# Optimization experiments

Measured on AMD Instinct MI355X. Metric: run time of the kernel, lower is better.

Reference implementation:

```python
import jax, jax.numpy as jnp
import numpy as np

N = 8192
N_DIM = 7
N_WIDTH = 64


def setup_inputs() -> dict:
    key = jax.random.key(0)
    ks = jax.random.split(key, 12)
    scale = 0.05
    u = lambda k, shape: scale * (2.0 * jax.random.uniform(k, shape) - 1.0)
    # Linear params stored as (in, out) so forward uses x @ W + b (same math as torch Linear).
    lin = lambda k, fan_in, fan_out: (
        jax.random.uniform(jax.random.fold_in(k, 0), (fan_in, fan_out),
                           minval=-1.0, maxval=1.0) / np.sqrt(fan_in),
        jax.random.uniform(jax.random.fold_in(k, 1), (fan_out,),
                           minval=-1.0, maxval=1.0) / np.sqrt(fan_in),
    )
    W1, b1 = lin(ks[1], N_DIM, N_WIDTH)
    W2, b2 = lin(ks[2], N_WIDTH, N_WIDTH)
    Wl, bl = lin(ks[3], N_WIDTH, 1)
    return {
        "x": jax.random.normal(ks[0], (N, N_DIM), dtype=jnp.float32),
        "alpha": jax.random.uniform(ks[4], (1,)),          # Edges.alpha = 1 * rand(1)
        "W1": W1, "b1": b1, "wt1": u(ks[5], (N_WIDTH, N_WIDTH)), "bs1": u(ks[6], (1,)),
        "W2": W2, "b2": b2, "wt2": u(ks[7], (N_WIDTH, N_WIDTH)), "bs2": u(ks[8], (1,)),
        "Wl": Wl, "bl": bl,
    }


def _edges(x, alpha):
    eta, phi = x[:, 1], x[:, 2]
    deta = eta[:, None] - eta[None, :]                      # (n, n)
    dphi = jnp.abs(phi[:, None] - phi[None, :])
    dphi = jnp.where(dphi > jnp.pi, 2.0 * jnp.pi - dphi, dphi)
    dRdR = deta * deta + dphi * dphi
    A = jnp.exp(-alpha[0] * dRdR)
    return jax.nn.softmax(A, axis=1) + jnp.eye(x.shape[0], dtype=x.dtype)


def _gcn_layer(X, A, W, b, wt, bs):
    X = jax.nn.relu(X @ W + b)                              # embed + relu
    X = (A @ X) @ wt + bs[0]                                # aggregate + mix + scalar bias
    return jax.nn.relu(X)


def reference(x, alpha, W1, b1, wt1, bs1, W2, b2, wt2, bs2, Wl, bl):
    A = _edges(x, alpha)
    V = jax.nn.relu(_gcn_layer(x, A, W1, b1, wt1, bs1))
    V = jax.nn.relu(_gcn_layer(V, A, W2, b2, wt2, bs2))
    s = V.sum(axis=0)                                       # (n_width,)
    return jax.nn.sigmoid(s @ Wl + bl)                      # (1,)
```

## Files before the change

### kernel.cpp

```cpp
#include <hip/hip_runtime.h>
#include <math.h>

#define NN 8192
#define L2E 1.44269504088896340736f
#define TWO_PI 6.28318530717958647693f

typedef _Float16 h8 __attribute__((ext_vector_type(8)));
typedef _Float16 h4 __attribute__((ext_vector_type(4)));
typedef float f32x4 __attribute__((ext_vector_type(4)));
#define MFMA16(A, B, C) __builtin_amdgcn_mfma_f32_16x16x32_f16(A, B, C, 0, 0, 0)

#define GLD_LDS16(gsrc, ldst)                                          \
  __builtin_amdgcn_global_load_lds(                                    \
      (const __attribute__((address_space(1))) unsigned int*)(gsrc),   \
      (__attribute__((address_space(3))) unsigned int*)(ldst), 16, 0, 0)

union V8 { float4 v[2]; float f[8]; };

__global__ __launch_bounds__(256) void prep_kernel(
    const float* __restrict__ x, const float* __restrict__ alpha,
    const float* __restrict__ W1, const float* __restrict__ b1,
    float* __restrict__ eta_s, float* __restrict__ phi_s,
    float* __restrict__ H1, _Float16* __restrict__ HT1,
    float* __restrict__ svec)
{
  __shared__ float sW[448];
  __shared__ float sb[64];
  __shared__ float T[32][65];
  const int t = threadIdx.x;
  if (blockIdx.x == 0 && t < 64) svec[t] = 0.f;
  for (int k = t; k < 448; k += 256) sW[k] = W1[k];
  if (t < 64) sb[t] = b1[t];
  const float s = sqrtf(alpha[0] * L2E);
  const int i0 = blockIdx.x * 32;
  const int r = t >> 3, q = t & 7;
  const int i = i0 + r;
  float xv[7];
#pragma unroll
  for (int k = 0; k < 7; k++) xv[k] = x[i * 7 + k];
  if (q == 0) { eta_s[i] = xv[1] * s; phi_s[i] = xv[2] * s; }
  __syncthreads();
#pragma unroll
  for (int c = 0; c < 8; c++) {
    const int n = q * 8 + c;
    float hv = sb[n];
#pragma unroll
    for (int k = 0; k < 7; k++) hv = fmaf(xv[k], sW[k * 64 + n], hv);
    T[r][n] = fmaxf(hv, 0.f);
  }
  __syncthreads();
  for (int e = t; e < 2048; e += 256) H1[i0 * 64 + e] = T[e >> 6][e & 63];
  const int n = t >> 2, sg = (t & 3) * 8;
  h8 v;
#pragma unroll
  for (int ss = 0; ss < 8; ss++) v[ss] = (_Float16)T[sg + ss][n];
  *(h8*)(HT1 + (size_t)n * NN + i0 + sg) = v;
}

template <bool NEED_L>
__global__ __launch_bounds__(256, 4) void attn_pass(
    const float* __restrict__ eta_s, const float* __restrict__ phi_s,
    const _Float16* __restrict__ HT, const float* __restrict__ alpha,
    float* __restrict__ Ypart, float* __restrict__ lpart)
{
  __shared__ __align__(16) char smem[33792];
  _Float16* stage = (_Float16*)smem;
  const int tid = threadIdx.x;
  const int w = tid >> 6, lane = tid & 63, m = lane & 15, g = lane >> 4;
  const int tile = blockIdx.x >> 2, part = blockIdx.x & 3;
  const int i0 = tile << 5;
  const int jbase = part << 11;
  const float Cs = TWO_PI * sqrtf(alpha[0] * L2E);
  const float et0 = eta_s[i0 + m],      ph0 = phi_s[i0 + m];
  const float et1 = eta_s[i0 + 16 + m], ph1 = phi_s[i0 + 16 + m];

  const int r0 = tid >> 4, gq = tid & 15;
  const _Float16* sbase = HT + (size_t)r0 * NN + ((gq ^ r0) << 3) + jbase;

  f32x4 a00 = {0,0,0,0}, a01 = {0,0,0,0}, a02 = {0,0,0,0}, a03 = {0,0,0,0};
  f32x4 a10 = {0,0,0,0}, a11 = {0,0,0,0}, a12 = {0,0,0,0}, a13 = {0,0,0,0};
  float l0 = 0.f, l1 = 0.f;

  const float* ep = eta_s + jbase + (w << 5) + (g << 3);
  const float* pp = phi_s + jbase + (w << 5) + (g << 3);
  V8 E, P, En, Pn;
  E.v[0] = *(const float4*)ep;  E.v[1] = *(const float4*)(ep + 4);
  P.v[0] = *(const float4*)pp;  P.v[1] = *(const float4*)(pp + 4);
  En = E; Pn = P;

#pragma unroll
  for (int k = 0; k < 4; ++k)
    GLD_LDS16(sbase + (size_t)k * 16 * NN, stage + ((k * 256 + tid) << 3));
  __syncthreads();

  const int fs = ((m << 4) + (((w << 2) | g) ^ m)) << 3;

  union AF { h8 v; decltype(__builtin_amdgcn_cvt_pkrtz(0.f, 0.f)) p[4]; };

  for (int s = 0; s < 16; ++s) {
    _Float16* cur = stage + ((s & 1) << 13);
    if (s < 15) {
      _Float16* nxt = stage + (((s + 1) & 1) << 13);
      const _Float16* srcp = sbase + (s + 1) * 128;
#pragma unroll
      for (int k = 0; k < 4; ++k)
        GLD_LDS16(srcp + (size_t)k * 16 * NN, nxt + ((k * 256 + tid) << 3));
      En.v[0] = *(const float4*)(ep + 128); En.v[1] = *(const float4*)(ep + 132);
      Pn.v[0] = *(const float4*)(pp + 128); Pn.v[1] = *(const float4*)(pp + 132);
      ep += 128; pp += 128;
    }
    const h8 b0 = *(const h8*)(cur + fs);
    const h8 b1 = *(const h8*)(cur + 2048 + fs);
    const h8 b2 = *(const h8*)(cur + 4096 + fs);
    const h8 b3 = *(const h8*)(cur + 6144 + fs);

    AF af0, af1;
#pragma unroll
    for (int tt = 0; tt < 8; tt += 2) {
      float Pv[4];
#pragma unroll
      for (int u = 0; u < 2; ++u) {
        {
          const float dp = ph0 - P.f[tt + u];
          const float ad = fabsf(dp);
          const float wr = fminf(ad, Cs - ad);
          const float de = et0 - E.f[tt + u];
          const float r2 = fmaf(de, de, wr * wr);
          const float a  = __builtin_amdgcn_exp2f(-r2);
          const float pv = __builtin_amdgcn_exp2f(fmaf(a, L2E, -L2E));
          if constexpr (NEED_L) l0 += pv;
          Pv[u] = pv;
        }
        {
          const float dp = ph1 - P.f[tt + u];
          const float ad = fabsf(dp);
          const float wr = fminf(ad, Cs - ad);
          const float de = et1 - E.f[tt + u];
          const float r2 = fmaf(de, de, wr * wr);
          const float a  = __builtin_amdgcn_exp2f(-r2);
          const float pv = __builtin_amdgcn_exp2f(fmaf(a, L2E, -L2E));
          if constexpr (NEED_L) l1 += pv;
          Pv[2 + u] = pv;
        }
      }
      af0.p[tt >> 1] = __builtin_amdgcn_cvt_pkrtz(Pv[0], Pv[1]);
      af1.p[tt >> 1] = __builtin_amdgcn_cvt_pkrtz(Pv[2], Pv[3]);
    }
    a00 = MFMA16(af0.v, b0, a00); a01 = MFMA16(af0.v, b1, a01);
    a02 = MFMA16(af0.v, b2, a02); a03 = MFMA16(af0.v, b3, a03);
    a10 = MFMA16(af1.v, b0, a10); a11 = MFMA16(af1.v, b1, a11);
    a12 = MFMA16(af1.v, b2, a12); a13 = MFMA16(af1.v, b3, a13);
    E = En; P = Pn;
    __syncthreads();
  }

  typedef float Red2[32][66];
  Red2* red = (Red2*)smem;
  float* lredF = (float*)(smem + 32768);
  const int h = w >> 1;
  if ((w & 1) == 0) {
#pragma unroll
    for (int r = 0; r < 4; ++r) {
      red[h][g * 4 + r][m]      = a00[r]; red[h][g * 4 + r][16 + m] = a01[r];
      red[h][g * 4 + r][32 + m] = a02[r]; red[h][g * 4 + r][48 + m] = a03[r];
      red[h][16 + g * 4 + r][m]      = a10[r]; red[h][16 + g * 4 + r][16 + m] = a11[r];
      red[h][16 + g * 4 + r][32 + m] = a12[r]; red[h][16 + g * 4 + r][48 + m] = a13[r];
    }
    if constexpr (NEED_L) {
      lredF[h * 128 + g * 32 + m] = l0; lredF[h * 128 + g * 32 + 16 + m] = l1;
    }
  }
  __syncthreads();
  if (w & 1) {
#pragma unroll
    for (int r = 0; r < 4; ++r) {
      red[h][g * 4 + r][m]      += a00[r]; red[h][g * 4 + r][16 + m] += a01[r];
      red[h][g * 4 + r][32 + m] += a02[r]; red[h][g * 4 + r][48 + m] += a03[r];
      red[h][16 + g * 4 + r][m]      += a10[r]; red[h][16 + g * 4 + r][16 + m] += a11[r];
      red[h][16 + g * 4 + r][32 + m] += a12[r]; red[h][16 + g * 4 + r][48 + m] += a13[r];
    }
    if constexpr (NEED_L) {
      lredF[h * 128 + g * 32 + m] += l0; lredF[h * 128 + g * 32 + 16 + m] += l1;
    }
  }
  __syncthreads();
#pragma unroll
  for (int k = 0; k < 8; ++k) {
    const int e = tid + k * 256;
    Ypart[((size_t)part * NN + i0 + (e >> 6)) * 64 + (e & 63)] =
        red[0][e >> 6][e & 63] + red[1][e >> 6][e & 63];
  }
  if constexpr (NEED_L) {
    if (tid < 32) {
      float sv = 0.f;
#pragma unroll
      for (int hh = 0; hh < 2; ++hh)
#pragma unroll
        for (int gg = 0; gg < 4; ++gg) sv += lredF[hh * 128 + gg * 32 + tid];
      lpart[(size_t)part * NN + i0 + tid] = sv;
    }
  }
}

__global__ __launch_bounds__(256) void mid_kernel(
    const float* __restrict__ Yp, const float* __restrict__ lp,
    const float* __restrict__ H1, const float* __restrict__ wt1,
    const float* __restrict__ bs1, const float* __restrict__ W2,
    const float* __restrict__ b2, float* __restrict__ H2,
    _Float16* __restrict__ HT2)
{
  __shared__ float sA[64][68];
  __shared__ float sB[64][68];
  __shared__ float U[16][65];
  __shared__ float sb2v[64];
  const int t = threadIdx.x;
  for (int e = t; e < 4096; e += 256) {
    sA[e >> 6][e & 63] = wt1[e];
    sB[e >> 6][e & 63] = W2[e];
  }
  if (t < 64) sb2v[t] = b2[t];
  const float bsv = bs1[0];
  const int i0 = blockIdx.x * 16;
  const int r = t >> 4, q = t & 15;
  const int i = i0 + r;
  float l = 0.f;
#pragma unroll
  for (int p = 0; p < 4; ++p) l += lp[(size_t)p * NN + i];
  const float rl = 1.0f / l;
  f32x4 ya = {0, 0, 0, 0};
#pragma unroll
  for (int p = 0; p < 4; ++p)
    ya += *(const f32x4*)(Yp + ((size_t)p * NN + i) * 64 + q * 4);
  const f32x4 h1 = *(const f32x4*)(H1 + (size_t)i * 64 + q * 4);
#pragma unroll
  for (int c = 0; c < 4; ++c) U[r][q * 4 + c] = fmaf(ya[c], rl, h1[c]);
  __syncthreads();
  float z[4];
#pragma unroll
  for (int c = 0; c < 4; ++c) z[c] = bsv;
  for (int k = 0; k < 64; ++k) {
    const float uk = U[r][k];
    const f32x4 sa = *(const f32x4*)&sA[k][q * 4];
#pragma unroll
    for (int c = 0; c < 4; ++c) z[c] = fmaf(uk, sa[c], z[c]);
  }
  __syncthreads();
#pragma unroll
  for (int c = 0; c < 4; ++c) U[r][q * 4 + c] = fmaxf(z[c], 0.f);
  __syncthreads();
  float hv[4];
#pragma unroll
  for (int c = 0; c < 4; ++c) hv[c] = sb2v[q * 4 + c];
  for (int k = 0; k < 64; ++k) {
    const float uk = U[r][k];
    const f32x4 sb4 = *(const f32x4*)&sB[k][q * 4];
#pragma unroll
    for (int c = 0; c < 4; ++c) hv[c] = fmaf(uk, sb4[c], hv[c]);
  }
  __syncthreads();
#pragma unroll
  for (int c = 0; c < 4; ++c) U[r][q * 4 + c] = fmaxf(hv[c], 0.f);
  __syncthreads();
  for (int e = t; e < 1024; e += 256) H2[i0 * 64 + e] = U[e >> 6][e & 63];
  const int n = t >> 2, sg = (t & 3) * 4;
  h4 v;
#pragma unroll
  for (int ss = 0; ss < 4; ss++) v[ss] = (_Float16)U[sg + ss][n];
  *(h4*)(HT2 + (size_t)n * NN + i0 + sg) = v;
}

__global__ __launch_bounds__(256) void final_kernel(
    const float* __restrict__ Yp, const float* __restrict__ lp,
    const float* __restrict__ H2, const float* __restrict__ wt2,
    const float* __restrict__ bs2, float* __restrict__ svec)
{
  __shared__ float sA[64][68];
  __shared__ float U[16][65];
  __shared__ float cred[4][64];
  const int t = threadIdx.x;
  for (int e = t; e < 4096; e += 256) sA[e >> 6][e & 63] = wt2[e];
  const float bsv = bs2[0];
  const int i0 = blockIdx.x * 16;
  const int r = t >> 4, q = t & 15;
  const int i = i0 + r;
  float l = 0.f;
#pragma unroll
  for (int p = 0; p < 4; ++p) l += lp[(size_t)p * NN + i];
  const float rl = 1.0f / l;
  f32x4 ya = {0, 0, 0, 0};
#pragma unroll
  for (int p = 0; p < 4; ++p)
    ya += *(const f32x4*)(Yp + ((size_t)p * NN + i) * 64 + q * 4);
  const f32x4 h2 = *(const f32x4*)(H2 + (size_t)i * 64 + q * 4);
#pragma unroll
  for (int c = 0; c < 4; ++c) U[r][q * 4 + c] = fmaf(ya[c], rl, h2[c]);
  __syncthreads();
  float z[4];
#pragma unroll
  for (int c = 0; c < 4; ++c) z[c] = bsv;
  for (int k = 0; k < 64; ++k) {
    const float uk = U[r][k];
    const f32x4 sa = *(const f32x4*)&sA[k][q * 4];
#pragma unroll
    for (int c = 0; c < 4; ++c) z[c] = fmaf(uk, sa[c], z[c]);
  }
  __syncthreads();
#pragma unroll
  for (int c = 0; c < 4; ++c) U[r][q * 4 + c] = fmaxf(z[c], 0.f);
  __syncthreads();
  const int col = t & 63, rg = t >> 6;
  float ps = 0.f;
#pragma unroll
  for (int rr = 0; rr < 4; rr++) ps += U[rg * 4 + rr][col];
  cred[rg][col] = ps;
  __syncthreads();
  if (t < 64)
    atomicAdd(svec + t, cred[0][t] + cred[1][t] + cred[2][t] + cred[3][t]);
}

__global__ void out_kernel(const float* __restrict__ svec,
                           const float* __restrict__ Wl,
                           const float* __restrict__ bl,
                           float* __restrict__ out)
{
  const int t = threadIdx.x;
  float v = svec[t] * Wl[t];
#pragma unroll
  for (int off = 32; off > 0; off >>= 1) v += __shfl_down(v, off);
  if (t == 0) {
    const float logit = v + bl[0];
    out[0] = 1.0f / (1.0f + __builtin_amdgcn_exp2f(-logit * L2E));
  }
}

extern "C" void kernel_launch(void* const* d_in, const int* in_sizes, int n_in,
                              void* d_out, int out_size, void* d_ws,
                              size_t ws_size, hipStream_t stream)
{
  const float* x     = (const float*)d_in[0];
  const float* alpha = (const float*)d_in[1];
  const float* W1    = (const float*)d_in[2];
  const float* b1    = (const float*)d_in[3];
  const float* wt1   = (const float*)d_in[4];
  const float* bs1   = (const float*)d_in[5];
  const float* W2    = (const float*)d_in[6];
  const float* b2    = (const float*)d_in[7];
  const float* wt2   = (const float*)d_in[8];
  const float* bs2   = (const float*)d_in[9];
  const float* Wl    = (const float*)d_in[10];
  const float* bl    = (const float*)d_in[11];
  float* out = (float*)d_out;

  char* ws = (char*)d_ws;
  size_t off = 0;
  auto alloc = [&](size_t bytes) {
    void* p = ws + off;
    off = (off + bytes + 255) & ~(size_t)255;
    return p;
  };
  float* eta_s = (float*)alloc(NN * 4 + 256);
  float* phi_s = (float*)alloc(NN * 4 + 256);
  float* H1    = (float*)alloc((size_t)NN * 64 * 4);
  float* H2    = (float*)alloc((size_t)NN * 64 * 4);
  float* Ypart = (float*)alloc((size_t)4 * NN * 64 * 4);
  float* lpart = (float*)alloc((size_t)4 * NN * 4);
  _Float16* HT = (_Float16*)alloc((size_t)NN * 64 * 2 + 512);
  float* svec  = (float*)alloc(64 * 4);

  prep_kernel<<<256, 256, 0, stream>>>(x, alpha, W1, b1, eta_s, phi_s, H1, HT, svec);
  attn_pass<true><<<1024, 256, 0, stream>>>(eta_s, phi_s, HT, alpha, Ypart, lpart);
  mid_kernel<<<512, 256, 0, stream>>>(Ypart, lpart, H1, wt1, bs1, W2, b2, H2, HT);
  attn_pass<false><<<1024, 256, 0, stream>>>(eta_s, phi_s, HT, alpha, Ypart, nullptr);
  final_kernel<<<512, 256, 0, stream>>>(Ypart, lpart, H2, wt2, bs2, svec);
  out_kernel<<<1, 64, 0, stream>>>(svec, Wl, bl, out);
}
```

Measured before the change: 172.9 us.

## Compute softmax row sums via MFMA, unroll attention pipeline, vectorize small kernels

The attention kernel now gets the softmax denominator from an extra MFMA of the probability fragment against a ones vector, replacing scalar accumulation. The per-element math is written with packed float2 vectors, and the double-buffered stage loop is unrolled by two with fixed buffers, dropping the lred scratch so shared memory is 32 KB. The prep, mid and final kernels use 16-byte vectorized global/LDS copies, padded tiles and unrolled inner GEMV loops. The ones-MFMA adds matrix work and sums fp16-rounded probabilities, which shifts the normalization precision slightly.

```diff
diff --git a/kernel.cpp b/kernel.cpp
--- a/kernel.cpp
+++ b/kernel.cpp
@@ -8,6 +8,7 @@
 typedef _Float16 h8 __attribute__((ext_vector_type(8)));
 typedef _Float16 h4 __attribute__((ext_vector_type(4)));
 typedef float f32x4 __attribute__((ext_vector_type(4)));
+typedef float f32x2 __attribute__((ext_vector_type(2)));
 #define MFMA16(A, B, C) __builtin_amdgcn_mfma_f32_16x16x32_f16(A, B, C, 0, 0, 0)
 
 #define GLD_LDS16(gsrc, ldst)                                          \
@@ -26,7 +27,7 @@
 {
   __shared__ float sW[448];
   __shared__ float sb[64];
-  __shared__ float T[32][65];
+  __shared__ float T[32][68];
   const int t = threadIdx.x;
   if (blockIdx.x == 0 && t < 64) svec[t] = 0.f;
   for (int k = t; k < 448; k += 256) sW[k] = W1[k];
@@ -49,7 +50,9 @@
     T[r][n] = fmaxf(hv, 0.f);
   }
   __syncthreads();
-  for (int e = t; e < 2048; e += 256) H1[i0 * 64 + e] = T[e >> 6][e & 63];
+  for (int e = t; e < 512; e += 256)
+    *(f32x4*)(H1 + (size_t)i0 * 64 + (e << 2)) =
+        *(const f32x4*)&T[e >> 4][(e << 2) & 63];
   const int n = t >> 2, sg = (t & 3) * 8;
   h8 v;
 #pragma unroll
@@ -63,7 +66,7 @@
     const _Float16* __restrict__ HT, const float* __restrict__ alpha,
     float* __restrict__ Ypart, float* __restrict__ lpart)
 {
-  __shared__ __align__(16) char smem[33792];
+  __shared__ __align__(16) char smem[32768];
   _Float16* stage = (_Float16*)smem;
   const int tid = threadIdx.x;
   const int w = tid >> 6, lane = tid & 63, m = lane & 15, g = lane >> 4;
@@ -79,14 +82,15 @@
 
   f32x4 a00 = {0,0,0,0}, a01 = {0,0,0,0}, a02 = {0,0,0,0}, a03 = {0,0,0,0};
   f32x4 a10 = {0,0,0,0}, a11 = {0,0,0,0}, a12 = {0,0,0,0}, a13 = {0,0,0,0};
-  float l0 = 0.f, l1 = 0.f;
+  f32x4 l0a = {0,0,0,0}, l1a = {0,0,0,0};
+  const h8 onesv = {(_Float16)1.f, (_Float16)1.f, (_Float16)1.f, (_Float16)1.f,
+                    (_Float16)1.f, (_Float16)1.f, (_Float16)1.f, (_Float16)1.f};
 
   const float* ep = eta_s + jbase + (w << 5) + (g << 3);
   const float* pp = phi_s + jbase + (w << 5) + (g << 3);
-  V8 E, P, En, Pn;
-  E.v[0] = *(const float4*)ep;  E.v[1] = *(const float4*)(ep + 4);
-  P.v[0] = *(const float4*)pp;  P.v[1] = *(const float4*)(pp + 4);
-  En = E; Pn = P;
+  V8 E0, P0, E1, P1;
+  E0.v[0] = *(const float4*)ep;  E0.v[1] = *(const float4*)(ep + 4);
+  P0.v[0] = *(const float4*)pp;  P0.v[1] = *(const float4*)(pp + 4);
 
 #pragma unroll
   for (int k = 0; k < 4; ++k)
@@ -97,66 +101,80 @@
 
   union AF { h8 v; decltype(__builtin_amdgcn_cvt_pkrtz(0.f, 0.f)) p[4]; };
 
-  for (int s = 0; s < 16; ++s) {
-    _Float16* cur = stage + ((s & 1) << 13);
-    if (s < 15) {
-      _Float16* nxt = stage + (((s + 1) & 1) << 13);
-      const _Float16* srcp = sbase + (s + 1) * 128;
-#pragma unroll
-      for (int k = 0; k < 4; ++k)
-        GLD_LDS16(srcp + (size_t)k * 16 * NN, nxt + ((k * 256 + tid) << 3));
-      En.v[0] = *(const float4*)(ep + 128); En.v[1] = *(const float4*)(ep + 132);
-      Pn.v[0] = *(const float4*)(pp + 128); Pn.v[1] = *(const float4*)(pp + 132);
-      ep += 128; pp += 128;
-    }
+  auto stage_compute = [&](const V8& Ec, const V8& Pc, const _Float16* cur) {
     const h8 b0 = *(const h8*)(cur + fs);
     const h8 b1 = *(const h8*)(cur + 2048 + fs);
     const h8 b2 = *(const h8*)(cur + 4096 + fs);
     const h8 b3 = *(const h8*)(cur + 6144 + fs);
-
     AF af0, af1;
 #pragma unroll
     for (int tt = 0; tt < 8; tt += 2) {
-      float Pv[4];
-#pragma unroll
-      for (int u = 0; u < 2; ++u) {
-        {
-          const float dp = ph0 - P.f[tt + u];
-          const float ad = fabsf(dp);
-          const float wr = fminf(ad, Cs - ad);
-          const float de = et0 - E.f[tt + u];
-          const float r2 = fmaf(de, de, wr * wr);
-          const float a  = __builtin_amdgcn_exp2f(-r2);
-          const float pv = __builtin_amdgcn_exp2f(fmaf(a, L2E, -L2E));
-          if constexpr (NEED_L) l0 += pv;
-          Pv[u] = pv;
-        }
-        {
-          const float dp = ph1 - P.f[tt + u];
-          const float ad = fabsf(dp);
-          const float wr = fminf(ad, Cs - ad);
-          const float de = et1 - E.f[tt + u];
-          const float r2 = fmaf(de, de, wr * wr);
-          const float a  = __builtin_amdgcn_exp2f(-r2);
-          const float pv = __builtin_amdgcn_exp2f(fmaf(a, L2E, -L2E));
-          if constexpr (NEED_L) l1 += pv;
-          Pv[2 + u] = pv;
-        }
-      }
-      af0.p[tt >> 1] = __builtin_amdgcn_cvt_pkrtz(Pv[0], Pv[1]);
-      af1.p[tt >> 1] = __builtin_amdgcn_cvt_pkrtz(Pv[2], Pv[3]);
+      const f32x2 pj = {Pc.f[tt], Pc.f[tt + 1]};
+      const f32x2 ej = {Ec.f[tt], Ec.f[tt + 1]};
+      const f32x2 dp0 = ph0 - pj, dp1 = ph1 - pj;
+      const f32x2 ad0 = {fabsf(dp0.x), fabsf(dp0.y)};
+      const f32x2 ad1 = {fabsf(dp1.x), fabsf(dp1.y)};
+      const f32x2 cm0 = Cs - ad0, cm1 = Cs - ad1;
+      const f32x2 wr0 = {fminf(ad0.x, cm0.x), fminf(ad0.y, cm0.y)};
+      const f32x2 wr1 = {fminf(ad1.x, cm1.x), fminf(ad1.y, cm1.y)};
+      const f32x2 de0 = et0 - ej, de1 = et1 - ej;
+      const f32x2 r20 = de0 * de0 + wr0 * wr0;
+      const f32x2 r21 = de1 * de1 + wr1 * wr1;
+      const f32x2 ax0 = {__builtin_amdgcn_exp2f(-r20.x),
+                         __builtin_amdgcn_exp2f(-r20.y)};
+      const f32x2 ax1 = {__builtin_amdgcn_exp2f(-r21.x),
+                         __builtin_amdgcn_exp2f(-r21.y)};
+      const f32x2 ga0 = ax0 * L2E - L2E;
+      const f32x2 ga1 = ax1 * L2E - L2E;
+      af0.p[tt >> 1] = __builtin_amdgcn_cvt_pkrtz(
+          __builtin_amdgcn_exp2f(ga0.x), __builtin_amdgcn_exp2f(ga0.y));
+      af1.p[tt >> 1] = __builtin_amdgcn_cvt_pkrtz(
+          __builtin_amdgcn_exp2f(ga1.x), __builtin_amdgcn_exp2f(ga1.y));
     }
     a00 = MFMA16(af0.v, b0, a00); a01 = MFMA16(af0.v, b1, a01);
     a02 = MFMA16(af0.v, b2, a02); a03 = MFMA16(af0.v, b3, a03);
     a10 = MFMA16(af1.v, b0, a10); a11 = MFMA16(af1.v, b1, a11);
     a12 = MFMA16(af1.v, b2, a12); a13 = MFMA16(af1.v, b3, a13);
-    E = En; P = Pn;
-    __syncthreads();
+    if constexpr (NEED_L) {
+      l0a = MFMA16(af0.v, onesv, l0a);
+      l1a = MFMA16(af1.v, onesv, l1a);
+    }
+  };
+
+#pragma unroll
+  for (int s2 = 0; s2 < 8; ++s2) {
+    {
+      const _Float16* src = sbase + (2 * s2 + 1) * 128;
+#pragma unroll
+      for (int k = 0; k < 4; ++k)
+        GLD_LDS16(src + (size_t)k * 16 * NN,
+                  stage + 8192 + ((k * 256 + tid) << 3));
+      E1.v[0] = *(const float4*)(ep + s2 * 256 + 128);
+      E1.v[1] = *(const float4*)(ep + s2 * 256 + 132);
+      P1.v[0] = *(const float4*)(pp + s2 * 256 + 128);
+      P1.v[1] = *(const float4*)(pp + s2 * 256 + 132);
+      stage_compute(E0, P0, stage);
+      __syncthreads();
+    }
+    {
+      if (s2 < 7) {
+        const _Float16* src = sbase + (2 * s2 + 2) * 128;
+#pragma unroll
+        for (int k = 0; k < 4; ++k)
+          GLD_LDS16(src + (size_t)k * 16 * NN,
+                    stage + ((k * 256 + tid) << 3));
+        E0.v[0] = *(const float4*)(ep + s2 * 256 + 256);
+        E0.v[1] = *(const float4*)(ep + s2 * 256 + 260);
+        P0.v[0] = *(const float4*)(pp + s2 * 256 + 256);
+        P0.v[1] = *(const float4*)(pp + s2 * 256 + 260);
+      }
+      stage_compute(E1, P1, stage + 8192);
+      __syncthreads();
+    }
   }
 
   typedef float Red2[32][66];
   Red2* red = (Red2*)smem;
-  float* lredF = (float*)(smem + 32768);
   const int h = w >> 1;
   if ((w & 1) == 0) {
 #pragma unroll
@@ -167,7 +185,13 @@
       red[h][16 + g * 4 + r][32 + m] = a12[r]; red[h][16 + g * 4 + r][48 + m] = a13[r];
     }
     if constexpr (NEED_L) {
-      lredF[h * 128 + g * 32 + m] = l0; lredF[h * 128 + g * 32 + 16 + m] = l1;
+      if (m == 0) {
+#pragma unroll
+        for (int r = 0; r < 4; ++r) {
+          red[h][g * 4 + r][64]      = l0a[r];
+          red[h][16 + g * 4 + r][64] = l1a[r];
+        }
+      }
     }
   }
   __syncthreads();
@@ -180,7 +204,13 @@
       red[h][16 + g * 4 + r][32 + m] += a12[r]; red[h][16 + g * 4 + r][48 + m] += a13[r];
     }
     if constexpr (NEED_L) {
-      lredF[h * 128 + g * 32 + m] += l0; lredF[h * 128 + g * 32 + 16 + m] += l1;
+      if (m == 0) {
+#pragma unroll
+        for (int r = 0; r < 4; ++r) {
+          red[h][g * 4 + r][64]      += l0a[r];
+          red[h][16 + g * 4 + r][64] += l1a[r];
+        }
+      }
     }
   }
   __syncthreads();
@@ -191,14 +221,8 @@
         red[0][e >> 6][e & 63] + red[1][e >> 6][e & 63];
   }
   if constexpr (NEED_L) {
-    if (tid < 32) {
-      float sv = 0.f;
-#pragma unroll
-      for (int hh = 0; hh < 2; ++hh)
-#pragma unroll
-        for (int gg = 0; gg < 4; ++gg) sv += lredF[hh * 128 + gg * 32 + tid];
-      lpart[(size_t)part * NN + i0 + tid] = sv;
-    }
+    if (tid < 32)
+      lpart[(size_t)part * NN + i0 + tid] = red[0][tid][64] + red[1][tid][64];
   }
 }
 
@@ -211,12 +235,13 @@
 {
   __shared__ float sA[64][68];
   __shared__ float sB[64][68];
-  __shared__ float U[16][65];
+  __shared__ float U[16][68];
   __shared__ float sb2v[64];
   const int t = threadIdx.x;
-  for (int e = t; e < 4096; e += 256) {
-    sA[e >> 6][e & 63] = wt1[e];
-    sB[e >> 6][e & 63] = W2[e];
+  for (int e = t; e < 1024; e += 256) {
+    const int rr = e >> 4, cc = (e << 2) & 63;
+    *(f32x4*)&sA[rr][cc] = *(const f32x4*)(wt1 + (e << 2));
+    *(f32x4*)&sB[rr][cc] = *(const f32x4*)(W2 + (e << 2));
   }
   if (t < 64) sb2v[t] = b2[t];
   const float bsv = bs1[0];
@@ -238,11 +263,15 @@
   float z[4];
 #pragma unroll
   for (int c = 0; c < 4; ++c) z[c] = bsv;
-  for (int k = 0; k < 64; ++k) {
-    const float uk = U[r][k];
-    const f32x4 sa = *(const f32x4*)&sA[k][q * 4];
-#pragma unroll
-    for (int c = 0; c < 4; ++c) z[c] = fmaf(uk, sa[c], z[c]);
+#pragma unroll
+  for (int k4 = 0; k4 < 64; k4 += 4) {
+    const f32x4 u4 = *(const f32x4*)&U[r][k4];
+#pragma unroll
+    for (int kk = 0; kk < 4; ++kk) {
+      const f32x4 sa = *(const f32x4*)&sA[k4 + kk][q * 4];
+#pragma unroll
+      for (int c = 0; c < 4; ++c) z[c] = fmaf(u4[kk], sa[c], z[c]);
+    }
   }
   __syncthreads();
 #pragma unroll
@@ -251,17 +280,22 @@
   float hv[4];
 #pragma unroll
   for (int c = 0; c < 4; ++c) hv[c] = sb2v[q * 4 + c];
-  for (int k = 0; k < 64; ++k) {
-    const float uk = U[r][k];
-    const f32x4 sb4 = *(const f32x4*)&sB[k][q * 4];
-#pragma unroll
-    for (int c = 0; c < 4; ++c) hv[c] = fmaf(uk, sb4[c], hv[c]);
+#pragma unroll
+  for (int k4 = 0; k4 < 64; k4 += 4) {
+    const f32x4 u4 = *(const f32x4*)&U[r][k4];
+#pragma unroll
+    for (int kk = 0; kk < 4; ++kk) {
+      const f32x4 sb4 = *(const f32x4*)&sB[k4 + kk][q * 4];
+#pragma unroll
+      for (int c = 0; c < 4; ++c) hv[c] = fmaf(u4[kk], sb4[c], hv[c]);
+    }
   }
   __syncthreads();
 #pragma unroll
   for (int c = 0; c < 4; ++c) U[r][q * 4 + c] = fmaxf(hv[c], 0.f);
   __syncthreads();
-  for (int e = t; e < 1024; e += 256) H2[i0 * 64 + e] = U[e >> 6][e & 63];
+  *(f32x4*)(H2 + (size_t)i0 * 64 + (t << 2)) =
+      *(const f32x4*)&U[t >> 4][(t << 2) & 63];
   const int n = t >> 2, sg = (t & 3) * 4;
   h4 v;
 #pragma unroll
@@ -275,10 +309,13 @@
     const float* __restrict__ bs2, float* __restrict__ svec)
 {
   __shared__ float sA[64][68];
-  __shared__ float U[16][65];
+  __shared__ float U[16][68];
   __shared__ float cred[4][64];
   const int t = threadIdx.x;
-  for (int e = t; e < 4096; e += 256) sA[e >> 6][e & 63] = wt2[e];
+  for (int e = t; e < 1024; e += 256) {
+    const int rr = e >> 4, cc = (e << 2) & 63;
+    *(f32x4*)&sA[rr][cc] = *(const f32x4*)(wt2 + (e << 2));
+  }
   const float bsv = bs2[0];
   const int i0 = blockIdx.x * 16;
   const int r = t >> 4, q = t & 15;
@@ -298,11 +335,15 @@
   float z[4];
 #pragma unroll
   for (int c = 0; c < 4; ++c) z[c] = bsv;
-  for (int k = 0; k < 64; ++k) {
-    const float uk = U[r][k];
-    const f32x4 sa = *(const f32x4*)&sA[k][q * 4];
-#pragma unroll
-    for (int c = 0; c < 4; ++c) z[c] = fmaf(uk, sa[c], z[c]);
+#pragma unroll
+  for (int k4 = 0; k4 < 64; k4 += 4) {
+    const f32x4 u4 = *(const f32x4*)&U[r][k4];
+#pragma unroll
+    for (int kk = 0; kk < 4; ++kk) {
+      const f32x4 sa = *(const f32x4*)&sA[k4 + kk][q * 4];
+#pragma unroll
+      for (int c = 0; c < 4; ++c) z[c] = fmaf(u4[kk], sa[c], z[c]);
+    }
   }
   __syncthreads();
 #pragma unroll
```

Result: faster. 168.3 us (-2.7%).
